# Performance work log

Hardware: AMD Instinct MI355X
Metric: run time of the kernel (lower is better)

Reference implementation:

```python
import jax, jax.numpy as jnp
import numpy as np

B, N, C, H = 4, 1024, 1024, 16
HD = C // H
SCALE = HD ** -0.5


def setup_inputs() -> dict:
    key = jax.random.key(0)
    ks = jax.random.split(key, 10)
    std = 0.02
    return {
        "x": jax.random.normal(ks[0], (B, N, C), dtype=jnp.float32),
        "voxel_coord": jax.random.uniform(ks[1], (B, N, 3), dtype=jnp.float32) * 50.0,
        "W_qk": jax.random.normal(ks[2], (2 * C, C), dtype=jnp.float32) * std,
        "W_v": jax.random.normal(ks[3], (C, C), dtype=jnp.float32) * std,
        "W_proj": jax.random.normal(ks[4], (C, C), dtype=jnp.float32) * std,
        "b_proj": jnp.zeros((C,), dtype=jnp.float32),
        "W_pos": jax.random.normal(ks[5], (H, 4), dtype=jnp.float32) * std,
        "b_pos": jnp.zeros((H,), dtype=jnp.float32),
        "gating": jnp.ones((H,), dtype=jnp.float32),
        "pos_emb": jax.random.normal(ks[6], (C, 3), dtype=jnp.float32),  # Embedding(max_points=dim, 3)
    }


def reference(x, voxel_coord, W_qk, W_v, W_proj, b_proj, W_pos, b_pos, gating, pos_emb):
    Bv, Nv, Cv = x.shape
    Hh = gating.shape[0]
    hd = Cv // Hh
    scale = hd ** -0.5

    # q, k, v  -> (B, H, N, hd)
    qk = (x @ W_qk.T).reshape(Bv, Nv, 2, Hh, hd).transpose(2, 0, 3, 1, 4)
    q, k = qk[0], qk[1]
    v = (x @ W_v.T).reshape(Bv, Nv, Hh, hd).transpose(0, 2, 1, 3)

    # relative 3D encodings: coords of embedding (broadcast over pairs) + pairwise distance
    rel = voxel_coord[:, :, None, :] - voxel_coord[:, None, :, :]        # (B,N,N,3)
    dist = jnp.sqrt(jnp.sum(rel * rel, axis=-1))                         # (B,N,N)
    pe = pos_emb[:Nv]                                                    # (N,3), arange(N) lookup
    pe_b = jnp.broadcast_to(pe[None, :, None, :], (Bv, Nv, Nv, 3))       # (B,N,N,3)
    enc = jnp.concatenate([pe_b, dist[..., None]], axis=-1)              # (B,N,N,4)

    # positional score path: Linear(4,H) -> softmax over keys -> @ V
    pos_logits = jnp.einsum('bnmf,hf->bhnm', enc, W_pos) + b_pos[None, :, None, None]
    pos_score = jax.nn.softmax(pos_logits, axis=-1)                      # (B,H,N,N)
    pos_out = jnp.einsum('bhnm,bhmd->bhnd', pos_score, v)                # (B,H,N,hd)

    # standard scaled dot-product attention path
    logits = jnp.einsum('bhnd,bhmd->bhnm', q, k) * scale
    patch_out = jnp.einsum('bhnm,bhmd->bhnd', jax.nn.softmax(logits, axis=-1), v)

    # sigmoid gate blend + renormalize over last (head_dim) axis, as in source
    g = jax.nn.sigmoid(gating)[None, :, None, None]
    attn = (1.0 - g) * patch_out + g * pos_out                           # (B,H,N,hd)
    attn = attn / jnp.sum(attn, axis=-1, keepdims=True)
    attn = attn.transpose(0, 2, 1, 3).reshape(Bv, Nv, Cv)

    return attn @ W_proj.T + b_proj
```

## Files before the change

### kernel.cpp

```cpp
#include <hip/hip_runtime.h>
#include <math.h>

#define B_ 4
#define N_ 1024
#define C_ 1024
#define H_ 16
#define HD_ 64

typedef float f32x2 __attribute__((ext_vector_type(2)));
typedef float f32x4 __attribute__((ext_vector_type(4)));
typedef short bf16x8 __attribute__((ext_vector_type(8)));

__device__ __forceinline__ unsigned short f2bf(float v) {
    unsigned u = __float_as_uint(v);
    u += 0x7FFFu + ((u >> 16) & 1u);
    return (unsigned short)(u >> 16);
}

__device__ __forceinline__ float bf2f(unsigned short h) {
    return __uint_as_float(((unsigned)h) << 16);
}

__device__ __forceinline__ float fast_exp2f(float x) {
#if __has_builtin(__builtin_amdgcn_exp2f)
    return __builtin_amdgcn_exp2f(x);
#else
    return exp2f(x);
#endif
}

__device__ __forceinline__ float rdfl(float v) {
    return __uint_as_float(__builtin_amdgcn_readfirstlane(__float_as_uint(v)));
}


__device__ __forceinline__ double fast_exp64(double a) {
    const double LOG2E = 1.4426950408889634074;
    const double LN2HI = 6.93147180369123816490e-01;
    const double LN2LO = 1.90821492927058770002e-10;
    const double MAGIC = 6755399441055744.0;
    double t     = a * LOG2E;
    double shift = t + MAGIC;
    int    n     = (int)__double_as_longlong(shift);
    double nd    = shift - MAGIC;
    double f     = __fma_rn(nd, -LN2HI, a);
    f            = __fma_rn(nd, -LN2LO, f);
    double p = 2.4801587301587301587e-05;
    p = __fma_rn(p, f, 1.9841269841269841270e-04);
    p = __fma_rn(p, f, 1.3888888888888888889e-03);
    p = __fma_rn(p, f, 8.3333333333333333333e-03);
    p = __fma_rn(p, f, 4.1666666666666666667e-02);
    p = __fma_rn(p, f, 1.6666666666666666667e-01);
    p = __fma_rn(p, f, 5.0e-01);
    p = __fma_rn(p, f, 1.0);
    p = __fma_rn(p, f, 1.0);
    return p * __longlong_as_double(((long long)(1023 + n)) << 52);
}

__global__ __launch_bounds__(256)
void cvt_bf16_kernel(const float* __restrict__ src, unsigned short* __restrict__ dst, int n)
{
    const int i = (blockIdx.x * 256 + threadIdx.x) * 8;
    if (i >= n) return;
    const float4 a = *reinterpret_cast<const float4*>(&src[i]);
    const float4 b = *reinterpret_cast<const float4*>(&src[i + 4]);
    unsigned short pk[8];
    pk[0] = f2bf(a.x); pk[1] = f2bf(a.y); pk[2] = f2bf(a.z); pk[3] = f2bf(a.w);
    pk[4] = f2bf(b.x); pk[5] = f2bf(b.y); pk[6] = f2bf(b.z); pk[7] = f2bf(b.w);
    *reinterpret_cast<bf16x8*>(&dst[i]) = *reinterpret_cast<bf16x8*>(pk);
}

__global__ __launch_bounds__(256)
void cvt_split_kernel(const float* __restrict__ src,
                      unsigned short* __restrict__ hi,
                      unsigned short* __restrict__ lo, int n)
{
    const int i = (blockIdx.x * 256 + threadIdx.x) * 8;
    if (i >= n) return;
    unsigned short ph[8], pl[8];
    #pragma unroll
    for (int j = 0; j < 8; ++j) {
        const float v = src[i + j];
        const unsigned short h = f2bf(v);
        ph[j] = h;
        pl[j] = f2bf(v - bf2f(h));
    }
    *reinterpret_cast<bf16x8*>(&hi[i]) = *reinterpret_cast<bf16x8*>(ph);
    *reinterpret_cast<bf16x8*>(&lo[i]) = *reinterpret_cast<bf16x8*>(pl);
}

__global__ __launch_bounds__(256)
void qk_split_kernel(const unsigned short* __restrict__ Ahi,
                     const unsigned short* __restrict__ Alo,
                     const unsigned short* __restrict__ Bhi,
                     const unsigned short* __restrict__ Blo,
                     float* __restrict__ outq,
                     float* __restrict__ outk,
                     int M, int O, int K)
{
    __shared__ unsigned short Ash[128][40];
    __shared__ unsigned short Asl[128][40];
    __shared__ unsigned short Bsh[64][40];
    __shared__ unsigned short Bsl[64][40];

    const int t  = threadIdx.x;
    const int w  = t >> 6;
    const int l  = t & 63;
    const int o0 = blockIdx.x * 64;
    const int m0 = blockIdx.y * 128;

    f32x4 acc[2][4];
    #pragma unroll
    for (int r = 0; r < 2; ++r)
        #pragma unroll
        for (int c = 0; c < 4; ++c) acc[r][c] = (f32x4){0.f, 0.f, 0.f, 0.f};

    const int ar = t >> 1, aseg = t & 1;
    const int br = t >> 2, bseg = t & 3;
    const int fr = l & 15, kg = l >> 4;

    for (int k0 = 0; k0 < K; k0 += 32) {
        const size_t abase = (size_t)(m0 + ar) * K + k0 + aseg * 16;
        const size_t bbase = (size_t)(o0 + br) * K + k0 + bseg * 8;
        const bf16x8 ah0 = *reinterpret_cast<const bf16x8*>(&Ahi[abase]);
        const bf16x8 ah1 = *reinterpret_cast<const bf16x8*>(&Ahi[abase + 8]);
        const bf16x8 al0 = *reinterpret_cast<const bf16x8*>(&Alo[abase]);
        const bf16x8 al1 = *reinterpret_cast<const bf16x8*>(&Alo[abase + 8]);
        const bf16x8 bh0 = *reinterpret_cast<const bf16x8*>(&Bhi[bbase]);
        const bf16x8 bl0 = *reinterpret_cast<const bf16x8*>(&Blo[bbase]);
        __syncthreads();
        *reinterpret_cast<bf16x8*>(&Ash[ar][aseg * 16])     = ah0;
        *reinterpret_cast<bf16x8*>(&Ash[ar][aseg * 16 + 8]) = ah1;
        *reinterpret_cast<bf16x8*>(&Asl[ar][aseg * 16])     = al0;
        *reinterpret_cast<bf16x8*>(&Asl[ar][aseg * 16 + 8]) = al1;
        *reinterpret_cast<bf16x8*>(&Bsh[br][bseg * 8])      = bh0;
        *reinterpret_cast<bf16x8*>(&Bsl[br][bseg * 8])      = bl0;
        __syncthreads();

        bf16x8 bfh[4], bfl[4];
        #pragma unroll
        for (int c = 0; c < 4; ++c) {
            bfh[c] = *reinterpret_cast<const bf16x8*>(&Bsh[c * 16 + fr][kg * 8]);
            bfl[c] = *reinterpret_cast<const bf16x8*>(&Bsl[c * 16 + fr][kg * 8]);
        }
        #pragma unroll
        for (int r = 0; r < 2; ++r) {
            const bf16x8 afh = *reinterpret_cast<const bf16x8*>(&Ash[w * 32 + r * 16 + fr][kg * 8]);
            const bf16x8 afl = *reinterpret_cast<const bf16x8*>(&Asl[w * 32 + r * 16 + fr][kg * 8]);
            #pragma unroll
            for (int c = 0; c < 4; ++c) {
                f32x4 a = acc[r][c];
                a = __builtin_amdgcn_mfma_f32_16x16x32_bf16(afh, bfh[c], a, 0, 0, 0);
                a = __builtin_amdgcn_mfma_f32_16x16x32_bf16(afh, bfl[c], a, 0, 0, 0);
                a = __builtin_amdgcn_mfma_f32_16x16x32_bf16(afl, bfh[c], a, 0, 0, 0);
                a = __builtin_amdgcn_mfma_f32_16x16x32_bf16(afl, bfl[c], a, 0, 0, 0);
                acc[r][c] = a;
            }
        }
    }

    #pragma unroll
    for (int c = 0; c < 4; ++c) {
        int oo = o0 + c * 16 + fr;
        float* dst = (oo < 1024) ? outq : outk;
        oo &= 1023;
        const int hh = oo >> 6, d0 = oo & 63;
        #pragma unroll
        for (int r = 0; r < 2; ++r) {
            #pragma unroll
            for (int j = 0; j < 4; ++j) {
                const int m = m0 + w * 32 + r * 16 + kg * 4 + j;
                const int bb_ = m >> 10, n = m & 1023;
                dst[((((size_t)bb_ * H_) + hh) * N_ + n) * HD_ + d0] = acc[r][c][j];
            }
        }
    }
}

template<int OUT_BF16>
__global__ __launch_bounds__(256)
void mfma_gemm_kernel(const unsigned short* __restrict__ A,
                      const unsigned short* __restrict__ Bw,
                      const float* __restrict__ bias,
                      float* __restrict__ outF,
                      unsigned short* __restrict__ outB,
                      int M, int O, int K)
{
    __shared__ unsigned short As[128][40];
    __shared__ unsigned short Bs[64][40];

    const int t  = threadIdx.x;
    const int w  = t >> 6;
    const int l  = t & 63;
    const int o0 = blockIdx.x * 64;
    const int m0 = blockIdx.y * 128;
    const size_t zoff = (size_t)blockIdx.z * 1048576;
    Bw += zoff;

    f32x4 acc[2][4];
    #pragma unroll
    for (int r = 0; r < 2; ++r)
        #pragma unroll
        for (int c = 0; c < 4; ++c) acc[r][c] = (f32x4){0.f, 0.f, 0.f, 0.f};

    const int ar = t >> 1, aseg = t & 1;
    const int br = t >> 2, bseg = t & 3;
    const int fr = l & 15, kg = l >> 4;

    for (int k0 = 0; k0 < K; k0 += 32) {
        const bf16x8 a0 = *reinterpret_cast<const bf16x8*>(&A[(size_t)(m0 + ar) * K + k0 + aseg * 16]);
        const bf16x8 a1 = *reinterpret_cast<const bf16x8*>(&A[(size_t)(m0 + ar) * K + k0 + aseg * 16 + 8]);
        const bf16x8 b0 = *reinterpret_cast<const bf16x8*>(&Bw[(size_t)(o0 + br) * K + k0 + bseg * 8]);
        __syncthreads();
        *reinterpret_cast<bf16x8*>(&As[ar][aseg * 16])     = a0;
        *reinterpret_cast<bf16x8*>(&As[ar][aseg * 16 + 8]) = a1;
        *reinterpret_cast<bf16x8*>(&Bs[br][bseg * 8])      = b0;
        __syncthreads();

        bf16x8 bfr[4];
        #pragma unroll
        for (int c = 0; c < 4; ++c)
            bfr[c] = *reinterpret_cast<const bf16x8*>(&Bs[c * 16 + fr][kg * 8]);
        #pragma unroll
        for (int r = 0; r < 2; ++r) {
            const bf16x8 af = *reinterpret_cast<const bf16x8*>(&As[w * 32 + r * 16 + fr][kg * 8]);
            #pragma unroll
            for (int c = 0; c < 4; ++c)
                acc[r][c] = __builtin_amdgcn_mfma_f32_16x16x32_bf16(af, bfr[c], acc[r][c], 0, 0, 0);
        }
    }

    #pragma unroll
    for (int c = 0; c < 4; ++c) {
        const int col = o0 + c * 16 + fr;
        const float bv = (OUT_BF16 == 0) ? bias[col] : 0.f;
        #pragma unroll
        for (int r = 0; r < 2; ++r) {
            #pragma unroll
            for (int j = 0; j < 4; ++j) {
                const int row = m0 + w * 32 + r * 16 + kg * 4 + j;
                const float v = acc[r][c][j] + bv;
                if (OUT_BF16)
                    outB[zoff + (size_t)row * O + col] = f2bf(v);
                else
                    outF[(size_t)row * O + col] = v;
            }
        }
    }
}

__global__ void wsum_kernel(const float* __restrict__ W_v, double* __restrict__ wsh)
{
    const int k = blockIdx.x * 256 + threadIdx.x;
    const int h = blockIdx.y;
    double s = 0.0;
    #pragma unroll 8
    for (int d = 0; d < 64; ++d) s += (double)W_v[(size_t)(h * 64 + d) * C_ + k];
    wsh[h * C_ + k] = s;
}

__global__ __launch_bounds__(256)
void vall_kernel(const float* __restrict__ x, const double* __restrict__ wsh,
                 double* __restrict__ Vall)
{
    __shared__ double ws_s[1024];
    const int h = blockIdx.y, b = blockIdx.z;
    const int m = blockIdx.x * 256 + threadIdx.x;
    for (int i = threadIdx.x; i < 1024; i += 256) ws_s[i] = wsh[h * C_ + i];
    __syncthreads();
    const float* xr = x + ((size_t)b * N_ + m) * C_;
    double acc = 0.0;
    #pragma unroll 8
    for (int kk = 0; kk < 1024; ++kk) acc += (double)xr[kk] * ws_s[kk];
    Vall[((size_t)b * H_ + h) * N_ + m] = acc;
}

__device__ __forceinline__ f32x2 pk_fma(f32x2 a, f32x2 b, f32x2 c) {
#if __has_builtin(__builtin_elementwise_fma)
    return __builtin_elementwise_fma(a, b, c);
#else
    f32x2 r; r.x = fmaf(a.x, b.x, c.x); r.y = fmaf(a.y, b.y, c.y); return r;
#endif
}

__global__ __launch_bounds__(256)
void attn_kernel(const float* __restrict__ q,
                 const float* __restrict__ k,
                 const unsigned short* __restrict__ vtb,
                 const double* __restrict__ Vall,
                 const float* __restrict__ coord,
                 const float* __restrict__ W_pos,
                 const float* __restrict__ gating,
                 unsigned short* __restrict__ attnB)
{
    __shared__ float4 Qs4[16][16];
    __shared__ float4 Kt4[64][16];
    __shared__ __align__(16) unsigned short ptB[16 * 64];
    __shared__ __align__(16) unsigned short qtB[16 * 64];
    __shared__ __align__(16) unsigned short VtB[2][64 * 64];

    const int t  = threadIdx.x;
    const int w  = t >> 6;
    const int l  = t & 63;
    const int n0 = blockIdx.x * 16;
    const int h  = blockIdx.y;
    const int b  = blockIdx.z;
    const size_t bhN = ((size_t)b * H_ + h) * N_;

    const int sr0 = t >> 4;
    const int sc  = t & 15;
    const int vd  = t >> 2;
    const int vkc = (t & 3) * 16;
    const unsigned short* vrow = vtb + (((size_t)b * H_ + h) * 64 + vd) * N_;
    const int vswz = (vd & 7) << 4;

    Qs4[t >> 4][t & 15] = reinterpret_cast<const float4*>(q + (bhN + n0) * HD_)[t];

    float qcx[4], qcy[4], qcz[4];
    #pragma unroll
    for (int i = 0; i < 4; ++i) {
        const float* cp = coord + ((size_t)b * N_ + n0 + w + 4 * i) * 3;
        qcx[i] = rdfl(cp[0]);
        qcy[i] = rdfl(cp[1]);
        qcz[i] = rdfl(cp[2]);
    }
    const double w4hd = (double)W_pos[h * 4 + 3];
    const double ghd  = 1.0 / (1.0 + exp(-(double)gating[h]));

    double sp[4], sq[4], spv[4], sqv[4];
    f32x4 accP = {0.f, 0.f, 0.f, 0.f};
    f32x4 accQ = {0.f, 0.f, 0.f, 0.f};
    #pragma unroll
    for (int i = 0; i < 4; ++i) { sp[i] = 0.0; sq[i] = 0.0; spv[i] = 0.0; sqv[i] = 0.0; }

    {
        const float4* kb4 = reinterpret_cast<const float4*>(k + bhN * HD_);
        #pragma unroll
        for (int i = 0; i < 4; ++i)
            Kt4[sr0 + i * 16][sc ^ ((sr0 + i * 16) & 15)] = kb4[t + i * 256];
        const bf16x8 v0 = *reinterpret_cast<const bf16x8*>(vrow + vkc);
        const bf16x8 v1 = *reinterpret_cast<const bf16x8*>(vrow + vkc + 8);
        char* vb = reinterpret_cast<char*>(&VtB[0][0]);
        *reinterpret_cast<bf16x8*>(vb + ((vd * 128 + vkc * 2)      ^ vswz)) = v0;
        *reinterpret_cast<bf16x8*>(vb + ((vd * 128 + vkc * 2 + 16) ^ vswz)) = v1;
    }
    double Vm  = Vall[bhN + l];
    double cmx = (double)coord[((size_t)b * N_ + l) * 3 + 0];
    double cmy = (double)coord[((size_t)b * N_ + l) * 3 + 1];
    double cmz = (double)coord[((size_t)b * N_ + l) * 3 + 2];
    __syncthreads();

    for (int t16 = 0; t16 < 16; ++t16) {
        const int m0   = t16 * 64;
        const int vcur = t16 & 1;

        float4 st0, st1, st2, st3;
        bf16x8 sv0, sv1;
        double VmN = 0.0, cmxN = 0.0, cmyN = 0.0, cmzN = 0.0;
        if (t16 < 15) {
            const float4* kb4 = reinterpret_cast<const float4*>(k + (bhN + m0 + 64) * HD_);
            st0 = kb4[t];
            st1 = kb4[t + 256];
            st2 = kb4[t + 512];
            st3 = kb4[t + 768];
            sv0 = *reinterpret_cast<const bf16x8*>(vrow + m0 + 64 + vkc);
            sv1 = *reinterpret_cast<const bf16x8*>(vrow + m0 + 64 + vkc + 8);
            VmN  = Vall[bhN + m0 + 64 + l];
            cmxN = (double)coord[((size_t)b * N_ + m0 + 64 + l) * 3 + 0];
            cmyN = (double)coord[((size_t)b * N_ + m0 + 64 + l) * 3 + 1];
            cmzN = (double)coord[((size_t)b * N_ + m0 + 64 + l) * 3 + 2];
        }

        f32x2 dot2[4][2];
        #pragma unroll
        for (int i = 0; i < 4; ++i) {
            dot2[i][0] = (f32x2){0.f, 0.f};
            dot2[i][1] = (f32x2){0.f, 0.f};
        }
        #pragma unroll
        for (int d4 = 0; d4 < 16; ++d4) {
            const float4 kt = Kt4[l][d4 ^ (l & 15)];
            const int g = d4 >> 3;
            const f32x2 kxy = {kt.x, kt.y};
            const f32x2 kzw = {kt.z, kt.w};
            #pragma unroll
            for (int i = 0; i < 4; ++i) {
                const float4 q4 = Qs4[w + 4 * i][d4];
                dot2[i][g] = pk_fma(kxy, (f32x2){q4.x, q4.y}, dot2[i][g]);
                dot2[i][g] = pk_fma(kzw, (f32x2){q4.z, q4.w}, dot2[i][g]);
            }
        }

        #pragma unroll
        for (int i = 0; i < 4; ++i) {
            const int r = w + 4 * i;
            const double lgs = (((double)dot2[i][0].x + (double)dot2[i][0].y) +
                                ((double)dot2[i][1].x + (double)dot2[i][1].y));
            const float pf = fast_exp2f((float)(lgs * 0.18033688011112042));
            const double dx = (double)qcx[i] - cmx;
            const double dy = (double)qcy[i] - cmy;
            const double dz = (double)qcz[i] - cmz;
            const double r2 = __fma_rn(dx, dx, __fma_rn(dy, dy, dz * dz));
            const double y0 = (double)rsqrtf((float)r2);
            const double y1 = y0 * __fma_rn(-0.5 * r2, y0 * y0, 1.5);
            const double dist = (r2 > 0.0) ? r2 * y1 : 0.0;
            const double q64 = fast_exp64(dist * w4hd);
            const int off = (r * 128 + l * 2) ^ ((r & 7) << 4);
            *reinterpret_cast<unsigned short*>(reinterpret_cast<char*>(ptB) + off) = f2bf(pf);
            *reinterpret_cast<unsigned short*>(reinterpret_cast<char*>(qtB) + off) = f2bf((float)q64);
            sp[i]  += (double)pf;
            sq[i]  += q64;
            spv[i] += (double)pf * Vm;
            sqv[i] += q64 * Vm;
        }
        __syncthreads();

        {
            const int r_   = l & 15;
            const int kb_  = l >> 4;
            const int aoff = r_ * 128 + kb_ * 16;
            const int aswz = (r_ & 7) << 4;
            const int dimw = w * 16 + r_;
            const int boff = dimw * 128 + kb_ * 16;
            const int bswz = (dimw & 7) << 4;
            const char* pbase = reinterpret_cast<const char*>(ptB);
            const char* qbase = reinterpret_cast<const char*>(qtB);
            const char* vbase = reinterpret_cast<const char*>(&VtB[vcur][0]);
            #pragma unroll
            for (int kh = 0; kh < 2; ++kh) {
                const bf16x8 afp = *reinterpret_cast<const bf16x8*>(pbase + ((aoff + kh * 64) ^ aswz));
                const bf16x8 afq = *reinterpret_cast<const bf16x8*>(qbase + ((aoff + kh * 64) ^ aswz));
                const bf16x8 bf_ = *reinterpret_cast<const bf16x8*>(vbase + ((boff + kh * 64) ^ bswz));
                accP = __builtin_amdgcn_mfma_f32_16x16x32_bf16(afp, bf_, accP, 0, 0, 0);
                accQ = __builtin_amdgcn_mfma_f32_16x16x32_bf16(afq, bf_, accQ, 0, 0, 0);
            }
        }

        if (t16 < 15) {
            Kt4[sr0     ][sc ^ ( sr0       & 15)] = st0;
            Kt4[sr0 + 16][sc ^ ((sr0 + 16) & 15)] = st1;
            Kt4[sr0 + 32][sc ^ ((sr0 + 32) & 15)] = st2;
            Kt4[sr0 + 48][sc ^ ((sr0 + 48) & 15)] = st3;
            char* vb = reinterpret_cast<char*>(&VtB[vcur ^ 1][0]);
            *reinterpret_cast<bf16x8*>(vb + ((vd * 128 + vkc * 2)      ^ vswz)) = sv0;
            *reinterpret_cast<bf16x8*>(vb + ((vd * 128 + vkc * 2 + 16) ^ vswz)) = sv1;
            Vm = VmN; cmx = cmxN; cmy = cmyN; cmz = cmzN;
        }
        __syncthreads();
    }

    double* epi = reinterpret_cast<double*>(ptB);
    #pragma unroll
    for (int i = 0; i < 4; ++i) {
        double vsp = sp[i], vsq = sq[i], vspv = spv[i], vsqv = sqv[i];
        #pragma unroll
        for (int mm = 32; mm >= 1; mm >>= 1) {
            vsp  += __shfl_xor(vsp,  mm);
            vsq  += __shfl_xor(vsq,  mm);
            vspv += __shfl_xor(vspv, mm);
            vsqv += __shfl_xor(vsqv, mm);
        }
        const double w1 = (1.0 - ghd) / vsp;
        const double w2 = ghd / vsq;
        if (l == 0) {
            epi[w + 4 * i]      = w1;
            epi[16 + w + 4 * i] = w2;
            epi[32 + w + 4 * i] = w1 * vspv + w2 * vsqv;
        }
    }
    __syncthreads();
    const int col = h * HD_ + w * 16 + (l & 15);
    #pragma unroll
    for (int j = 0; j < 4; ++j) {
        const int m = 4 * (l >> 4) + j;
        const double a = epi[m] * (double)accP[j] + epi[16 + m] * (double)accQ[j];
        attnB[((size_t)b * N_ + n0 + m) * C_ + col] = f2bf((float)(a / epi[32 + m]));
    }
}

extern "C" void kernel_launch(void* const* d_in, const int* in_sizes, int n_in,
                              void* d_out, int out_size, void* d_ws, size_t ws_size,
                              hipStream_t stream)
{
    const float* x      = (const float*)d_in[0];
    const float* coord  = (const float*)d_in[1];
    const float* W_qk   = (const float*)d_in[2];
    const float* W_v    = (const float*)d_in[3];
    const float* W_proj = (const float*)d_in[4];
    const float* b_proj = (const float*)d_in[5];
    const float* W_pos  = (const float*)d_in[6];
    const float* gating = (const float*)d_in[8];

    float* ws   = (float*)d_ws;
    const size_t per = (size_t)B_ * H_ * N_ * HD_;
    float*          qb    = ws;
    float*          kb    = qb + per;
    unsigned short* attnB = (unsigned short*)(kb + per);
    unsigned short* WqkHi = attnB;
    unsigned short* WqkLo = attnB + 2 * (size_t)C_ * C_;
    unsigned short* vtb   = attnB + per;
    unsigned short* xhi   = vtb + per;
    unsigned short* xlo   = xhi + per;
    unsigned short* WvB   = xlo + per;
    unsigned short* WpB   = WvB + (size_t)C_ * C_;
    double*         wsh   = (double*)(WpB + (size_t)C_ * C_);
    double*         Vall  = wsh + (size_t)H_ * C_;
    float*          out   = (float*)d_out;

    cvt_split_kernel<<<2048, 256, 0, stream>>>(x, xhi, xlo, (int)per);
    cvt_split_kernel<<<1024, 256, 0, stream>>>(W_qk, WqkHi, WqkLo, 2 * C_ * C_);
    cvt_bf16_kernel<<<512, 256, 0, stream>>>(W_v, WvB, C_ * C_);
    cvt_bf16_kernel<<<512, 256, 0, stream>>>(W_proj, WpB, C_ * C_);

    wsum_kernel<<<dim3(4, 16), 256, 0, stream>>>(W_v, wsh);
    vall_kernel<<<dim3(4, 16, 4), 256, 0, stream>>>(x, wsh, Vall);

    qk_split_kernel<<<dim3(32, 32), 256, 0, stream>>>(
        xhi, xlo, WqkHi, WqkLo, qb, kb, B_ * N_, 2 * C_, C_);

    mfma_gemm_kernel<1><<<dim3(16, 8, 4), 256, 0, stream>>>(
        WvB, xhi, nullptr, nullptr, vtb, C_, N_, C_);

    attn_kernel<<<dim3(N_ / 16, H_, B_), 256, 0, stream>>>(
        qb, kb, vtb, Vall, coord, W_pos, gating, attnB);

    mfma_gemm_kernel<0><<<dim3(16, 32, 1), 256, 0, stream>>>(
        attnB, WpB, b_proj, out, nullptr, B_ * N_, C_, C_);
}
```

Measured before the change: 544.7 us.

## Double attention query tile to 32 rows with 512-thread blocks

The attention kernel now processes 32 query rows per block using 8 waves instead of 16 rows with 4 waves, so each K/V tile loaded into shared memory serves twice as many queries. The goal is to halve global K/V traffic per query and the per-thread staging loads. In exchange the grid has half as many blocks, each using more LDS and threads, which can lower occupancy or leave the GPU less evenly filled.

```diff
diff --git a/kernel.cpp b/kernel.cpp
--- a/kernel.cpp
+++ b/kernel.cpp
@@ -283,7 +283,7 @@
 #endif
 }
 
-__global__ __launch_bounds__(256)
+__global__ __launch_bounds__(512)
 void attn_kernel(const float* __restrict__ q,
                  const float* __restrict__ k,
                  const unsigned short* __restrict__ vtb,
@@ -293,24 +293,24 @@
                  const float* __restrict__ gating,
                  unsigned short* __restrict__ attnB)
 {
-    __shared__ float4 Qs4[16][16];
+    __shared__ float4 Qs4[32][16];
     __shared__ float4 Kt4[64][16];
-    __shared__ __align__(16) unsigned short ptB[16 * 64];
-    __shared__ __align__(16) unsigned short qtB[16 * 64];
+    __shared__ __align__(16) unsigned short ptB[32 * 64];
+    __shared__ __align__(16) unsigned short qtB[32 * 64];
     __shared__ __align__(16) unsigned short VtB[2][64 * 64];
 
     const int t  = threadIdx.x;
     const int w  = t >> 6;
     const int l  = t & 63;
-    const int n0 = blockIdx.x * 16;
+    const int n0 = blockIdx.x * 32;
     const int h  = blockIdx.y;
     const int b  = blockIdx.z;
     const size_t bhN = ((size_t)b * H_ + h) * N_;
 
     const int sr0 = t >> 4;
     const int sc  = t & 15;
-    const int vd  = t >> 2;
-    const int vkc = (t & 3) * 16;
+    const int vd   = t >> 3;
+    const int vko  = (t & 7) * 16;
     const unsigned short* vrow = vtb + (((size_t)b * H_ + h) * 64 + vd) * N_;
     const int vswz = (vd & 7) << 4;
 
@@ -319,7 +319,7 @@
     float qcx[4], qcy[4], qcz[4];
     #pragma unroll
     for (int i = 0; i < 4; ++i) {
-        const float* cp = coord + ((size_t)b * N_ + n0 + w + 4 * i) * 3;
+        const float* cp = coord + ((size_t)b * N_ + n0 + w + 8 * i) * 3;
         qcx[i] = rdfl(cp[0]);
         qcy[i] = rdfl(cp[1]);
         qcz[i] = rdfl(cp[2]);
@@ -335,14 +335,11 @@
 
     {
         const float4* kb4 = reinterpret_cast<const float4*>(k + bhN * HD_);
-        #pragma unroll
-        for (int i = 0; i < 4; ++i)
-            Kt4[sr0 + i * 16][sc ^ ((sr0 + i * 16) & 15)] = kb4[t + i * 256];
-        const bf16x8 v0 = *reinterpret_cast<const bf16x8*>(vrow + vkc);
-        const bf16x8 v1 = *reinterpret_cast<const bf16x8*>(vrow + vkc + 8);
+        Kt4[sr0     ][sc ^ ( sr0       & 15)] = kb4[t];
+        Kt4[sr0 + 32][sc ^ ((sr0 + 32) & 15)] = kb4[t + 512];
+        const bf16x8 v0 = *reinterpret_cast<const bf16x8*>(vrow + (t & 7) * 8);
         char* vb = reinterpret_cast<char*>(&VtB[0][0]);
-        *reinterpret_cast<bf16x8*>(vb + ((vd * 128 + vkc * 2)      ^ vswz)) = v0;
-        *reinterpret_cast<bf16x8*>(vb + ((vd * 128 + vkc * 2 + 16) ^ vswz)) = v1;
+        *reinterpret_cast<bf16x8*>(vb + ((vd * 128 + vko) ^ vswz)) = v0;
     }
     double Vm  = Vall[bhN + l];
     double cmx = (double)coord[((size_t)b * N_ + l) * 3 + 0];
@@ -354,17 +351,14 @@
         const int m0   = t16 * 64;
         const int vcur = t16 & 1;
 
-        float4 st0, st1, st2, st3;
-        bf16x8 sv0, sv1;
+        float4 st0, st1;
+        bf16x8 sv0;
         double VmN = 0.0, cmxN = 0.0, cmyN = 0.0, cmzN = 0.0;
         if (t16 < 15) {
             const float4* kb4 = reinterpret_cast<const float4*>(k + (bhN + m0 + 64) * HD_);
             st0 = kb4[t];
-            st1 = kb4[t + 256];
-            st2 = kb4[t + 512];
-            st3 = kb4[t + 768];
-            sv0 = *reinterpret_cast<const bf16x8*>(vrow + m0 + 64 + vkc);
-            sv1 = *reinterpret_cast<const bf16x8*>(vrow + m0 + 64 + vkc + 8);
+            st1 = kb4[t + 512];
+            sv0 = *reinterpret_cast<const bf16x8*>(vrow + m0 + 64 + (t & 7) * 8);
             VmN  = Vall[bhN + m0 + 64 + l];
             cmxN = (double)coord[((size_t)b * N_ + m0 + 64 + l) * 3 + 0];
             cmyN = (double)coord[((size_t)b * N_ + m0 + 64 + l) * 3 + 1];
@@ -385,7 +379,7 @@
             const f32x2 kzw = {kt.z, kt.w};
             #pragma unroll
             for (int i = 0; i < 4; ++i) {
-                const float4 q4 = Qs4[w + 4 * i][d4];
+                const float4 q4 = Qs4[w + 8 * i][d4];
                 dot2[i][g] = pk_fma(kxy, (f32x2){q4.x, q4.y}, dot2[i][g]);
                 dot2[i][g] = pk_fma(kzw, (f32x2){q4.z, q4.w}, dot2[i][g]);
             }
@@ -393,7 +387,7 @@
 
         #pragma unroll
         for (int i = 0; i < 4; ++i) {
-            const int r = w + 4 * i;
+            const int r = w + 8 * i;
             const double lgs = (((double)dot2[i][0].x + (double)dot2[i][0].y) +
                                 ((double)dot2[i][1].x + (double)dot2[i][1].y));
             const float pf = fast_exp2f((float)(lgs * 0.18033688011112042));
@@ -416,13 +410,14 @@
         __syncthreads();
 
         {
-            const int r_   = l & 15;
-            const int kb_  = l >> 4;
-            const int aoff = r_ * 128 + kb_ * 16;
-            const int aswz = (r_ & 7) << 4;
-            const int dimw = w * 16 + r_;
-            const int boff = dimw * 128 + kb_ * 16;
-            const int bswz = (dimw & 7) << 4;
+            const int r_    = l & 15;
+            const int kb_   = l >> 4;
+            const int arow  = (w >> 2) * 16 + r_;
+            const int aoff  = arow * 128 + kb_ * 16;
+            const int aswz  = (r_ & 7) << 4;
+            const int dimw  = (w & 3) * 16 + r_;
+            const int boff  = dimw * 128 + kb_ * 16;
+            const int bswz  = (dimw & 7) << 4;
             const char* pbase = reinterpret_cast<const char*>(ptB);
             const char* qbase = reinterpret_cast<const char*>(qtB);
             const char* vbase = reinterpret_cast<const char*>(&VtB[vcur][0]);
@@ -438,12 +433,9 @@
 
         if (t16 < 15) {
             Kt4[sr0     ][sc ^ ( sr0       & 15)] = st0;
-            Kt4[sr0 + 16][sc ^ ((sr0 + 16) & 15)] = st1;
-            Kt4[sr0 + 32][sc ^ ((sr0 + 32) & 15)] = st2;
-            Kt4[sr0 + 48][sc ^ ((sr0 + 48) & 15)] = st3;
+            Kt4[sr0 + 32][sc ^ ((sr0 + 32) & 15)] = st1;
             char* vb = reinterpret_cast<char*>(&VtB[vcur ^ 1][0]);
-            *reinterpret_cast<bf16x8*>(vb + ((vd * 128 + vkc * 2)      ^ vswz)) = sv0;
-            *reinterpret_cast<bf16x8*>(vb + ((vd * 128 + vkc * 2 + 16) ^ vswz)) = sv1;
+            *reinterpret_cast<bf16x8*>(vb + ((vd * 128 + vko) ^ vswz)) = sv0;
             Vm = VmN; cmx = cmxN; cmy = cmyN; cmz = cmzN;
         }
         __syncthreads();
@@ -463,18 +455,19 @@
         const double w1 = (1.0 - ghd) / vsp;
         const double w2 = ghd / vsq;
         if (l == 0) {
-            epi[w + 4 * i]      = w1;
-            epi[16 + w + 4 * i] = w2;
-            epi[32 + w + 4 * i] = w1 * vspv + w2 * vsqv;
+            const int r = w + 8 * i;
+            epi[r]      = w1;
+            epi[32 + r] = w2;
+            epi[64 + r] = w1 * vspv + w2 * vsqv;
         }
     }
     __syncthreads();
-    const int col = h * HD_ + w * 16 + (l & 15);
+    const int col = h * HD_ + (w & 3) * 16 + (l & 15);
     #pragma unroll
     for (int j = 0; j < 4; ++j) {
-        const int m = 4 * (l >> 4) + j;
-        const double a = epi[m] * (double)accP[j] + epi[16 + m] * (double)accQ[j];
-        attnB[((size_t)b * N_ + n0 + m) * C_ + col] = f2bf((float)(a / epi[32 + m]));
+        const int m = (w >> 2) * 16 + 4 * (l >> 4) + j;
+        const double a = epi[m] * (double)accP[j] + epi[32 + m] * (double)accQ[j];
+        attnB[((size_t)b * N_ + n0 + m) * C_ + col] = f2bf((float)(a / epi[64 + m]));
     }
 }
 
@@ -521,7 +514,7 @@
     mfma_gemm_kernel<1><<<dim3(16, 8, 4), 256, 0, stream>>>(
         WvB, xhi, nullptr, nullptr, vtb, C_, N_, C_);
 
-    attn_kernel<<<dim3(N_ / 16, H_, B_), 256, 0, stream>>>(
+    attn_kernel<<<dim3(N_ / 32, H_, B_), 512, 0, stream>>>(
         qb, kb, vtb, Vall, coord, W_pos, gating, attnB);
 
     mfma_gemm_kernel<0><<<dim3(16, 32, 1), 256, 0, stream>>>(
```

Measured after the change: 552.3 us. No clear change (+1.4%).

## Precompute pairwise distances once per batch instead of per head in attention

Applied to the files above, without the earlier changes.

Adds a dist_kernel that computes the N×N fp64 pairwise distance matrix for two batches at a time into reused workspace (aliasing the xhi/xlo buffers). The attention kernel then loads the distances instead of recomputing sqrt for every head, removing 16× redundant fp64 work. In exchange it adds 8 MB-per-batch-pair of global reads per head and splits the attention launch into two halves, which may lower occupancy and add launch overhead.

```diff
diff --git a/kernel.cpp b/kernel.cpp
--- a/kernel.cpp
+++ b/kernel.cpp
@@ -27,10 +27,6 @@
 #else
     return exp2f(x);
 #endif
-}
-
-__device__ __forceinline__ float rdfl(float v) {
-    return __uint_as_float(__builtin_amdgcn_readfirstlane(__float_as_uint(v)));
 }
 
 
@@ -58,6 +54,25 @@
 }
 
 __global__ __launch_bounds__(256)
+void dist_kernel(const float* __restrict__ coord, double* __restrict__ dist,
+                 int bbase)
+{
+    const int m = blockIdx.x * 256 + threadIdx.x;
+    const int n = blockIdx.y;
+    const int z = blockIdx.z;
+    const int b = bbase + z;
+    const float* cq = coord + ((size_t)b * N_ + n) * 3;
+    const float* cm = coord + ((size_t)b * N_ + m) * 3;
+    const double dx = (double)cq[0] - (double)cm[0];
+    const double dy = (double)cq[1] - (double)cm[1];
+    const double dz = (double)cq[2] - (double)cm[2];
+    const double r2 = __fma_rn(dx, dx, __fma_rn(dy, dy, dz * dz));
+    const double y0 = (double)rsqrtf((float)r2);
+    const double y1 = y0 * __fma_rn(-0.5 * r2, y0 * y0, 1.5);
+    dist[((size_t)z * N_ + n) * N_ + m] = (r2 > 0.0) ? r2 * y1 : 0.0;
+}
+
+__global__ __launch_bounds__(256)
 void cvt_bf16_kernel(const float* __restrict__ src, unsigned short* __restrict__ dst, int n)
 {
     const int i = (blockIdx.x * 256 + threadIdx.x) * 8;
@@ -288,10 +303,11 @@
                  const float* __restrict__ k,
                  const unsigned short* __restrict__ vtb,
                  const double* __restrict__ Vall,
-                 const float* __restrict__ coord,
+                 const double* __restrict__ dist,
                  const float* __restrict__ W_pos,
                  const float* __restrict__ gating,
-                 unsigned short* __restrict__ attnB)
+                 unsigned short* __restrict__ attnB,
+                 int bbase)
 {
     __shared__ float4 Qs4[16][16];
     __shared__ float4 Kt4[64][16];
@@ -304,7 +320,8 @@
     const int l  = t & 63;
     const int n0 = blockIdx.x * 16;
     const int h  = blockIdx.y;
-    const int b  = blockIdx.z;
+    const int z  = blockIdx.z;
+    const int b  = bbase + z;
     const size_t bhN = ((size_t)b * H_ + h) * N_;
 
     const int sr0 = t >> 4;
@@ -314,16 +331,12 @@
     const unsigned short* vrow = vtb + (((size_t)b * H_ + h) * 64 + vd) * N_;
     const int vswz = (vd & 7) << 4;
 
+    const double* dr0 = dist + ((size_t)z * N_ + n0 + w     ) * N_;
+    const double* dr1 = dist + ((size_t)z * N_ + n0 + w + 4 ) * N_;
+    const double* dr2 = dist + ((size_t)z * N_ + n0 + w + 8 ) * N_;
+    const double* dr3 = dist + ((size_t)z * N_ + n0 + w + 12) * N_;
+
     Qs4[t >> 4][t & 15] = reinterpret_cast<const float4*>(q + (bhN + n0) * HD_)[t];
-
-    float qcx[4], qcy[4], qcz[4];
-    #pragma unroll
-    for (int i = 0; i < 4; ++i) {
-        const float* cp = coord + ((size_t)b * N_ + n0 + w + 4 * i) * 3;
-        qcx[i] = rdfl(cp[0]);
-        qcy[i] = rdfl(cp[1]);
-        qcz[i] = rdfl(cp[2]);
-    }
     const double w4hd = (double)W_pos[h * 4 + 3];
     const double ghd  = 1.0 / (1.0 + exp(-(double)gating[h]));
 
@@ -344,10 +357,8 @@
         *reinterpret_cast<bf16x8*>(vb + ((vd * 128 + vkc * 2)      ^ vswz)) = v0;
         *reinterpret_cast<bf16x8*>(vb + ((vd * 128 + vkc * 2 + 16) ^ vswz)) = v1;
     }
-    double Vm  = Vall[bhN + l];
-    double cmx = (double)coord[((size_t)b * N_ + l) * 3 + 0];
-    double cmy = (double)coord[((size_t)b * N_ + l) * 3 + 1];
-    double cmz = (double)coord[((size_t)b * N_ + l) * 3 + 2];
+    double Vm = Vall[bhN + l];
+    double dv0 = dr0[l], dv1 = dr1[l], dv2 = dr2[l], dv3 = dr3[l];
     __syncthreads();
 
     for (int t16 = 0; t16 < 16; ++t16) {
@@ -356,7 +367,7 @@
 
         float4 st0, st1, st2, st3;
         bf16x8 sv0, sv1;
-        double VmN = 0.0, cmxN = 0.0, cmyN = 0.0, cmzN = 0.0;
+        double VmN = 0.0, dN0 = 0.0, dN1 = 0.0, dN2 = 0.0, dN3 = 0.0;
         if (t16 < 15) {
             const float4* kb4 = reinterpret_cast<const float4*>(k + (bhN + m0 + 64) * HD_);
             st0 = kb4[t];
@@ -365,10 +376,11 @@
             st3 = kb4[t + 768];
             sv0 = *reinterpret_cast<const bf16x8*>(vrow + m0 + 64 + vkc);
             sv1 = *reinterpret_cast<const bf16x8*>(vrow + m0 + 64 + vkc + 8);
-            VmN  = Vall[bhN + m0 + 64 + l];
-            cmxN = (double)coord[((size_t)b * N_ + m0 + 64 + l) * 3 + 0];
-            cmyN = (double)coord[((size_t)b * N_ + m0 + 64 + l) * 3 + 1];
-            cmzN = (double)coord[((size_t)b * N_ + m0 + 64 + l) * 3 + 2];
+            VmN = Vall[bhN + m0 + 64 + l];
+            dN0 = dr0[m0 + 64 + l];
+            dN1 = dr1[m0 + 64 + l];
+            dN2 = dr2[m0 + 64 + l];
+            dN3 = dr3[m0 + 64 + l];
         }
 
         f32x2 dot2[4][2];
@@ -391,20 +403,14 @@
             }
         }
 
+        const double dvs[4] = {dv0, dv1, dv2, dv3};
         #pragma unroll
         for (int i = 0; i < 4; ++i) {
             const int r = w + 4 * i;
             const double lgs = (((double)dot2[i][0].x + (double)dot2[i][0].y) +
                                 ((double)dot2[i][1].x + (double)dot2[i][1].y));
             const float pf = fast_exp2f((float)(lgs * 0.18033688011112042));
-            const double dx = (double)qcx[i] - cmx;
-            const double dy = (double)qcy[i] - cmy;
-            const double dz = (double)qcz[i] - cmz;
-            const double r2 = __fma_rn(dx, dx, __fma_rn(dy, dy, dz * dz));
-            const double y0 = (double)rsqrtf((float)r2);
-            const double y1 = y0 * __fma_rn(-0.5 * r2, y0 * y0, 1.5);
-            const double dist = (r2 > 0.0) ? r2 * y1 : 0.0;
-            const double q64 = fast_exp64(dist * w4hd);
+            const double q64 = fast_exp64(dvs[i] * w4hd);
             const int off = (r * 128 + l * 2) ^ ((r & 7) << 4);
             *reinterpret_cast<unsigned short*>(reinterpret_cast<char*>(ptB) + off) = f2bf(pf);
             *reinterpret_cast<unsigned short*>(reinterpret_cast<char*>(qtB) + off) = f2bf((float)q64);
@@ -444,7 +450,7 @@
             char* vb = reinterpret_cast<char*>(&VtB[vcur ^ 1][0]);
             *reinterpret_cast<bf16x8*>(vb + ((vd * 128 + vkc * 2)      ^ vswz)) = sv0;
             *reinterpret_cast<bf16x8*>(vb + ((vd * 128 + vkc * 2 + 16) ^ vswz)) = sv1;
-            Vm = VmN; cmx = cmxN; cmy = cmyN; cmz = cmzN;
+            Vm = VmN; dv0 = dN0; dv1 = dN1; dv2 = dN2; dv3 = dN3;
         }
         __syncthreads();
     }
@@ -501,6 +507,7 @@
     unsigned short* vtb   = attnB + per;
     unsigned short* xhi   = vtb + per;
     unsigned short* xlo   = xhi + per;
+    double*         distB = (double*)xhi;
     unsigned short* WvB   = xlo + per;
     unsigned short* WpB   = WvB + (size_t)C_ * C_;
     double*         wsh   = (double*)(WpB + (size_t)C_ * C_);
@@ -521,8 +528,13 @@
     mfma_gemm_kernel<1><<<dim3(16, 8, 4), 256, 0, stream>>>(
         WvB, xhi, nullptr, nullptr, vtb, C_, N_, C_);
 
-    attn_kernel<<<dim3(N_ / 16, H_, B_), 256, 0, stream>>>(
-        qb, kb, vtb, Vall, coord, W_pos, gating, attnB);
+    dist_kernel<<<dim3(4, 1024, 2), 256, 0, stream>>>(coord, distB, 0);
+    attn_kernel<<<dim3(N_ / 16, H_, 2), 256, 0, stream>>>(
+        qb, kb, vtb, Vall, distB, W_pos, gating, attnB, 0);
+
+    dist_kernel<<<dim3(4, 1024, 2), 256, 0, stream>>>(coord, distB, 2);
+    attn_kernel<<<dim3(N_ / 16, H_, 2), 256, 0, stream>>>(
+        qb, kb, vtb, Vall, distB, W_pos, gating, attnB, 2);
 
     mfma_gemm_kernel<0><<<dim3(16, 32, 1), 256, 0, stream>>>(
         attnB, WpB, b_proj, out, nullptr, B_ * N_, C_, C_);
```

New measurement: 552.7 us. About the same (+1.5%).
